# Performance work log

Hardware: AMD Instinct MI355X
Metric: run time of the kernel (lower is better)

Reference implementation:

```python
import jax, jax.numpy as jnp
import numpy as np

EPS = 1e-5

def _bn_relu(x, g, b, m, v):
    # inference batchnorm + relu, NCHW, fused affine
    scale = g * jax.lax.rsqrt(v + EPS)
    shift = b - m * scale
    return jnp.maximum(x * scale[None, :, None, None] + shift[None, :, None, None], 0.0)

def _conv1x1(x, w):
    # x: [B,C,H,W], w: [O,C]
    return jnp.einsum('bchw,oc->bohw', x, w)

def _xcorr_depthwise(search, kernel, padding=0):
    # search: [B,C,Hs,Ws], kernel: [B,C,Hk,Wk]; grouped conv, groups=B*C
    B, C, Hs, Ws = search.shape
    Hk, Wk = kernel.shape[2], kernel.shape[3]
    x = search.reshape(1, B * C, Hs, Ws)
    k = kernel.reshape(B * C, 1, Hk, Wk)
    out = jax.lax.conv_general_dilated(
        x, k, window_strides=(1, 1), padding=[(padding, padding), (padding, padding)],
        feature_group_count=B * C, dimension_numbers=('NCHW', 'OIHW', 'NCHW'))
    return out.reshape(B, C, out.shape[2], out.shape[3])

def setup_inputs():
    key = jax.random.key(0)
    ks = jax.random.split(key, 20)
    B, Cin, HID, COUT = 128, 256, 256, 20
    s = 1.0 / np.sqrt(Cin)
    inp = {
        'kernel': jax.random.normal(ks[0], (B, Cin, 7, 7), jnp.float32),
        'search': jax.random.normal(ks[1], (B, Cin, 31, 31), jnp.float32),
        # conv_kernel branch (1x1 conv weight stored as [O,C]) + BN stats
        'w_k': jax.random.normal(ks[2], (HID, Cin), jnp.float32) * s,
        'g_k': 1.0 + 0.1 * jax.random.normal(ks[3], (HID,), jnp.float32),
        'b_k': 0.1 * jax.random.normal(ks[4], (HID,), jnp.float32),
        'm_k': 0.1 * jax.random.normal(ks[5], (HID,), jnp.float32),
        'v_k': jax.random.uniform(ks[6], (HID,), jnp.float32, 0.5, 1.5),
        # conv_search branch
        'w_s': jax.random.normal(ks[7], (HID, Cin), jnp.float32) * s,
        'g_s': 1.0 + 0.1 * jax.random.normal(ks[8], (HID,), jnp.float32),
        'b_s': 0.1 * jax.random.normal(ks[9], (HID,), jnp.float32),
        'm_s': 0.1 * jax.random.normal(ks[10], (HID,), jnp.float32),
        'v_s': jax.random.uniform(ks[11], (HID,), jnp.float32, 0.5, 1.5),
        # head: conv1(1x1)+BN+ReLU, conv2(1x1, bias)
        'w_h1': jax.random.normal(ks[12], (HID, HID), jnp.float32) * (1.0 / np.sqrt(HID)),
        'g_h': 1.0 + 0.1 * jax.random.normal(ks[13], (HID,), jnp.float32),
        'b_h': 0.1 * jax.random.normal(ks[14], (HID,), jnp.float32),
        'm_h': 0.1 * jax.random.normal(ks[15], (HID,), jnp.float32),
        'v_h': jax.random.uniform(ks[16], (HID,), jnp.float32, 0.5, 1.5),
        'w_h2': jax.random.normal(ks[17], (COUT, HID), jnp.float32) * (1.0 / np.sqrt(HID)),
        'bias_h2': 0.1 * jax.random.normal(ks[18], (COUT,), jnp.float32),
    }
    return inp

def reference(kernel, search, w_k, g_k, b_k, m_k, v_k, w_s, g_s, b_s, m_s, v_s,
              w_h1, g_h, b_h, m_h, v_h, w_h2, bias_h2):
    k = _bn_relu(_conv1x1(kernel, w_k), g_k, b_k, m_k, v_k)   # [B,256,7,7]
    s = _bn_relu(_conv1x1(search, w_s), g_s, b_s, m_s, v_s)   # [B,256,31,31]
    feat = _xcorr_depthwise(s, k, padding=0)                  # [B,256,25,25]
    y = _bn_relu(_conv1x1(feat, w_h1), g_h, b_h, m_h, v_h)
    out = _conv1x1(y, w_h2) + bias_h2[None, :, None, None]    # [B,20,25,25]
    return out
```

## Files before the change

### kernel.cpp

```cpp
#include <hip/hip_runtime.h>
#include <hip/hip_fp16.h>

typedef _Float16 f16;
typedef __attribute__((ext_vector_type(8))) _Float16 f16x8;
typedef __attribute__((ext_vector_type(4))) _Float16 f16x4;
typedef __attribute__((ext_vector_type(4))) float f32x4;

#define MFMA16(a, b, c) __builtin_amdgcn_mfma_f32_16x16x32_f16((a), (b), (c), 0, 0, 0)

#define OFF_WK   0u
#define OFF_WS   131072u
#define OFF_WH1  262144u
#define OFF_W2P  393216u
#define OFF_SH   409600u
#define OFF_S    412672u
#define OFF_KF   63392768u
#define OFF_FEAT 66604032u

__global__ __launch_bounds__(256) void prep_weights(
    const float* __restrict__ wk, const float* __restrict__ gk, const float* __restrict__ bk,
    const float* __restrict__ mk, const float* __restrict__ vk,
    const float* __restrict__ wsr, const float* __restrict__ gs, const float* __restrict__ bs,
    const float* __restrict__ ms, const float* __restrict__ vs,
    const float* __restrict__ wh1, const float* __restrict__ gh, const float* __restrict__ bh,
    const float* __restrict__ mh, const float* __restrict__ vh,
    const float* __restrict__ wh2,
    f16* __restrict__ wk16, f16* __restrict__ ws16, f16* __restrict__ wh116,
    f16* __restrict__ w2p, float* __restrict__ shifts) {
  int o = blockIdx.x;
  int t = threadIdx.x;
  float sck = gk[o] * rsqrtf(vk[o] + 1e-5f);
  float scs = gs[o] * rsqrtf(vs[o] + 1e-5f);
  float sch = gh[o] * rsqrtf(vh[o] + 1e-5f);
  int idx = o * 256 + t;
  wk16[idx]  = (f16)(wk[idx] * sck);
  ws16[idx]  = (f16)(wsr[idx] * scs);
  wh116[idx] = (f16)(wh1[idx] * sch);
  if (o < 32) w2p[idx] = (o < 20) ? (f16)wh2[idx] : (f16)0;
  if (t == 0) {
    shifts[o]       = bk[o] - mk[o] * sck;
    shifts[256 + o] = bs[o] - ms[o] * scs;
    shifts[512 + o] = bh[o] - mh[o] * sch;
  }
}

__global__ __launch_bounds__(256) void conv_f32_allo(
    const float* __restrict__ X, const f16* __restrict__ W,
    const float* __restrict__ shift, f16* __restrict__ out,
    int P, int CP ) {
  const int C = 256;
  int n0 = blockIdx.x * 64;
  int t = threadIdx.x;
  int lane = t & 63, wave = t >> 6;
  int fm = lane & 15, kg = lane >> 4;

  __shared__ f16 Bs[32][64][8];

  {
    int n = t & 63;
    int cblk = t >> 6;
    int gn = n0 + n;
    int bq = gn / P, bp = gn - bq * P;
    const float* xcol = X + (size_t)bq * CP + bp;
#pragma unroll
    for (int j = 0; j < 8; ++j) {
      int cbase = cblk * 64 + j * 8;
      const float* xp = xcol + (size_t)cbase * P;
      f16x8 v;
#pragma unroll
      for (int e = 0; e < 8; ++e) v[e] = (f16)xp[(size_t)e * P];
      *(f16x8*)&Bs[cbase >> 3][n][0] = v;
    }
  }
  __syncthreads();

  const f16* wp = W + (size_t)(wave * 64 + fm) * C + kg * 8;

  f32x4 acc[4][4] = {};
#pragma unroll
  for (int c0 = 0; c0 < 256; c0 += 32) {
    f16x8 a[4], b[4];
#pragma unroll
    for (int of = 0; of < 4; ++of) a[of] = *(const f16x8*)(wp + (size_t)of * 16 * C + c0);
#pragma unroll
    for (int nf = 0; nf < 4; ++nf) b[nf] = *(const f16x8*)&Bs[(c0 >> 3) + kg][nf * 16 + fm][0];
#pragma unroll
    for (int of = 0; of < 4; ++of)
#pragma unroll
      for (int nf = 0; nf < 4; ++nf)
        acc[of][nf] = MFMA16(a[of], b[nf], acc[of][nf]);
  }

#pragma unroll
  for (int of = 0; of < 4; ++of) {
    int orow = wave * 64 + of * 16 + kg * 4;
#pragma unroll
    for (int nf = 0; nf < 4; ++nf) {
      int n = n0 + nf * 16 + fm;
      f16x4 st;
#pragma unroll
      for (int r = 0; r < 4; ++r)
        st[r] = (f16)fmaxf(acc[of][nf][r] + shift[orow + r], 0.0f);
      *(f16x4*)&out[(size_t)n * 256 + orow] = st;
    }
  }
}

__global__ __launch_bounds__(256) void xcorr_dw_row(
    const f16* __restrict__ S ,
    const f16* __restrict__ K ,
    f16* __restrict__ F ) {
  int id = blockIdx.x;
  int x = id & 7;
  int r = id >> 3;
  int g = r % 7;
  int bq = r / 7;
  int b = bq * 8 + x;

  int wave = threadIdx.x >> 6;
  int lane = threadIdx.x & 63;
  int oi = g * 4 + wave;
  if (oi >= 25) return;

  const f16* Sb = S + (size_t)b * 961 * 256 + lane * 4;
  const f16* Kb = K + (size_t)b * 49 * 256 + lane * 4;

  f32x4 acc[25] = {};

  for (int di = 0; di < 7; ++di) {
    const f16* sp = Sb + (size_t)(oi + di) * 31 * 256;
    f16x4 srow[31];
#pragma unroll
    for (int j = 0; j < 31; ++j) srow[j] = *(const f16x4*)(sp + (size_t)j * 256);
    const f16* kp = Kb + (size_t)di * 7 * 256;
    f16x4 krow[7];
#pragma unroll
    for (int j = 0; j < 7; ++j) krow[j] = *(const f16x4*)(kp + (size_t)j * 256);

#pragma unroll
    for (int dj = 0; dj < 7; ++dj) {
      float k0 = (float)krow[dj][0];
      float k1 = (float)krow[dj][1];
      float k2 = (float)krow[dj][2];
      float k3 = (float)krow[dj][3];
#pragma unroll
      for (int oj = 0; oj < 25; ++oj) {
        f16x4 sv = srow[oj + dj];
        acc[oj][0] += (float)sv[0] * k0;
        acc[oj][1] += (float)sv[1] * k1;
        acc[oj][2] += (float)sv[2] * k2;
        acc[oj][3] += (float)sv[3] * k3;
      }
    }
  }

  f16* Fb = F + ((size_t)b * 625 + (size_t)oi * 25) * 256 + lane * 4;
#pragma unroll
  for (int oj = 0; oj < 25; ++oj) {
    f16x4 o;
#pragma unroll
    for (int e = 0; e < 4; ++e) o[e] = (f16)acc[oj][e];
    *(f16x4*)(Fb + (size_t)oj * 256) = o;
  }
}

__global__ __launch_bounds__(256) void head_fused(
    const f16* __restrict__ Xt ,
    const f16* __restrict__ W1, const float* __restrict__ shift,
    const f16* __restrict__ W2p , const float* __restrict__ bias,
    float* __restrict__ out ) {
  const int C = 256;
  int n0 = blockIdx.x * 64;
  int t = threadIdx.x;
  int lane = t & 63, wave = t >> 6;
  int fm = lane & 15, kg = lane >> 4;

  __shared__ f16 Ys[32][64][8];

  const f16* wp = W1 + (size_t)(wave * 64 + fm) * C + kg * 8;
  const f16* xp = Xt + (size_t)(n0 + fm) * C + kg * 8;

  f32x4 acc[4][4] = {};
#pragma unroll
  for (int c0 = 0; c0 < 256; c0 += 32) {
    f16x8 a[4], b[4];
#pragma unroll
    for (int of = 0; of < 4; ++of) a[of] = *(const f16x8*)(wp + (size_t)of * 16 * C + c0);
#pragma unroll
    for (int nf = 0; nf < 4; ++nf) b[nf] = *(const f16x8*)(xp + (size_t)nf * 16 * C + c0);
#pragma unroll
    for (int of = 0; of < 4; ++of)
#pragma unroll
      for (int nf = 0; nf < 4; ++nf)
        acc[of][nf] = MFMA16(a[of], b[nf], acc[of][nf]);
  }

#pragma unroll
  for (int of = 0; of < 4; ++of) {
    int orow = wave * 64 + of * 16 + kg * 4;
#pragma unroll
    for (int nf = 0; nf < 4; ++nf) {
      int n = nf * 16 + fm;
      f16x4 st;
#pragma unroll
      for (int r = 0; r < 4; ++r)
        st[r] = (f16)fmaxf(acc[of][nf][r] + shift[orow + r], 0.0f);
      *(f16x4*)&Ys[orow >> 3][n][(kg & 1) * 4] = st;
    }
  }
  __syncthreads();

  f32x4 acc2[2] = {};
#pragma unroll
  for (int c0 = 0; c0 < 256; c0 += 32) {
    f16x8 b = *(const f16x8*)&Ys[(c0 >> 3) + kg][wave * 16 + fm][0];
    f16x8 a0 = *(const f16x8*)(W2p + (size_t)fm * C + c0 + kg * 8);
    f16x8 a1 = *(const f16x8*)(W2p + (size_t)(16 + fm) * C + c0 + kg * 8);
    acc2[0] = MFMA16(a0, b, acc2[0]);
    acc2[1] = MFMA16(a1, b, acc2[1]);
  }

  int n = n0 + wave * 16 + fm;
  int bq = n / 625, bp = n - bq * 625;
  float* op = out + (size_t)bq * 12500 + bp;
#pragma unroll
  for (int of = 0; of < 2; ++of) {
#pragma unroll
    for (int r = 0; r < 4; ++r) {
      int o = of * 16 + kg * 4 + r;
      if (o < 20) op[(size_t)o * 625] = acc2[of][r] + bias[o];
    }
  }
}

extern "C" void kernel_launch(void* const* d_in, const int* in_sizes, int n_in,
                              void* d_out, int out_size, void* d_ws, size_t ws_size,
                              hipStream_t stream) {
  const float* kernel_in = (const float*)d_in[0];
  const float* search    = (const float*)d_in[1];
  const float* w_k = (const float*)d_in[2];
  const float* g_k = (const float*)d_in[3];
  const float* b_k = (const float*)d_in[4];
  const float* m_k = (const float*)d_in[5];
  const float* v_k = (const float*)d_in[6];
  const float* w_s = (const float*)d_in[7];
  const float* g_s = (const float*)d_in[8];
  const float* b_s = (const float*)d_in[9];
  const float* m_s = (const float*)d_in[10];
  const float* v_s = (const float*)d_in[11];
  const float* w_h1 = (const float*)d_in[12];
  const float* g_h = (const float*)d_in[13];
  const float* b_h = (const float*)d_in[14];
  const float* m_h = (const float*)d_in[15];
  const float* v_h = (const float*)d_in[16];
  const float* w_h2 = (const float*)d_in[17];
  const float* bias_h2 = (const float*)d_in[18];
  float* out = (float*)d_out;

  char* ws = (char*)d_ws;
  f16* wk16  = (f16*)(ws + OFF_WK);
  f16* ws16  = (f16*)(ws + OFF_WS);
  f16* wh116 = (f16*)(ws + OFF_WH1);
  f16* w2p   = (f16*)(ws + OFF_W2P);
  float* shifts = (float*)(ws + OFF_SH);
  f16* sbuf = (f16*)(ws + OFF_S);
  f16* kbuf = (f16*)(ws + OFF_KF);
  f16* fbuf = (f16*)(ws + OFF_FEAT);

  prep_weights<<<256, 256, 0, stream>>>(w_k, g_k, b_k, m_k, v_k,
                                        w_s, g_s, b_s, m_s, v_s,
                                        w_h1, g_h, b_h, m_h, v_h, w_h2,
                                        wk16, ws16, wh116, w2p, shifts);

  conv_f32_allo<<<dim3(1922), 256, 0, stream>>>(
      search, ws16, shifts + 256, sbuf, 961, 256 * 961);

  conv_f32_allo<<<dim3(98), 256, 0, stream>>>(
      kernel_in, wk16, shifts + 0, kbuf, 49, 256 * 49);

  xcorr_dw_row<<<dim3(896), 256, 0, stream>>>(sbuf, kbuf, fbuf);

  head_fused<<<dim3(1250), 256, 0, stream>>>(
      fbuf, wh116, shifts + 512, w2p, bias_h2, out);
}
```

Measured before the change: 184.0 us.

## Split 1x1 conv into channel-last f16 transpose plus in-place MFMA GEMM

Replaces the fused f32-load-and-convert 1x1 conv with two steps. A templated transpose kernel converts NCHW f32 input to channel-last f16 using vectorized loads. A GEMM kernel then reads the channel-last data straight from global memory without LDS staging, uses a wider 128-column tile and writes its result in place. The aim is cheaper, more coalesced loads and better MFMA reuse, but it adds an extra write and read of the intermediate f16 tensor in global memory.

Measured after the change: 216.4 us. +17.6%, slower.

```diff
diff --git a/kernel.cpp b/kernel.cpp
--- a/kernel.cpp
+++ b/kernel.cpp
@@ -44,64 +44,83 @@
   }
 }
 
-__global__ __launch_bounds__(256) void conv_f32_allo(
-    const float* __restrict__ X, const f16* __restrict__ W,
-    const float* __restrict__ shift, f16* __restrict__ out,
-    int P, int CP ) {
+template <int P>
+__global__ __launch_bounds__(256) void transpose_cl(
+    const float* __restrict__ X, f16* __restrict__ out) {
+  int p0 = blockIdx.x * 128;
+  int c0 = blockIdx.y * 64;
+  int b  = blockIdx.z;
+  int t = threadIdx.x;
+  int cg = t & 7;
+  int pq = t >> 3;
+  int p = p0 + pq * 4;
+  if (p >= P) return;
+  const float* xb = X + ((size_t)b * 256 + c0 + cg * 8) * P;
+  f32x4 col[8];
+  if (p + 3 < P) {
+#pragma unroll
+    for (int j = 0; j < 8; ++j) col[j] = *(const f32x4*)(xb + (size_t)j * P + p);
+  } else {
+#pragma unroll
+    for (int j = 0; j < 8; ++j)
+#pragma unroll
+      for (int e = 0; e < 4; ++e)
+        col[j][e] = (p + e < P) ? xb[(size_t)j * P + p + e] : 0.0f;
+  }
+#pragma unroll
+  for (int e = 0; e < 4; ++e) {
+    if (p + e < P) {
+      f16x8 v;
+#pragma unroll
+      for (int j = 0; j < 8; ++j) v[j] = (f16)col[j][e];
+      *(f16x8*)(out + ((size_t)b * P + p + e) * 256 + c0 + cg * 8) = v;
+    }
+  }
+}
+
+__global__ __launch_bounds__(256, 2) void gemm_cl(
+    const f16* Xt, const f16* __restrict__ W,
+    const float* __restrict__ shift, f16* out) {
   const int C = 256;
-  int n0 = blockIdx.x * 64;
+  int n0 = blockIdx.x * 128;
   int t = threadIdx.x;
   int lane = t & 63, wave = t >> 6;
   int fm = lane & 15, kg = lane >> 4;
 
-  __shared__ f16 Bs[32][64][8];
-
-  {
-    int n = t & 63;
-    int cblk = t >> 6;
-    int gn = n0 + n;
-    int bq = gn / P, bp = gn - bq * P;
-    const float* xcol = X + (size_t)bq * CP + bp;
-#pragma unroll
-    for (int j = 0; j < 8; ++j) {
-      int cbase = cblk * 64 + j * 8;
-      const float* xp = xcol + (size_t)cbase * P;
-      f16x8 v;
-#pragma unroll
-      for (int e = 0; e < 8; ++e) v[e] = (f16)xp[(size_t)e * P];
-      *(f16x8*)&Bs[cbase >> 3][n][0] = v;
-    }
-  }
+  const f16* wp = W + (size_t)(wave * 64 + fm) * C + kg * 8;
+  const f16* xp = Xt + (size_t)(n0 + fm) * C + kg * 8;
+
+  f32x4 acc[4][8] = {};
+#pragma unroll
+  for (int ci = 0; ci < 8; ++ci) {
+    f16x8 b[8], a[4];
+#pragma unroll
+    for (int nf = 0; nf < 8; ++nf)
+      b[nf] = *(const f16x8*)(xp + (size_t)nf * 16 * C + ci * 32);
+#pragma unroll
+    for (int of = 0; of < 4; ++of)
+      a[of] = *(const f16x8*)(wp + (size_t)of * 16 * C + ci * 32);
+#pragma unroll
+    for (int of = 0; of < 4; ++of)
+#pragma unroll
+      for (int nf = 0; nf < 8; ++nf)
+        acc[of][nf] = MFMA16(a[of], b[nf], acc[of][nf]);
+  }
+
   __syncthreads();
-
-  const f16* wp = W + (size_t)(wave * 64 + fm) * C + kg * 8;
-
-  f32x4 acc[4][4] = {};
-#pragma unroll
-  for (int c0 = 0; c0 < 256; c0 += 32) {
-    f16x8 a[4], b[4];
-#pragma unroll
-    for (int of = 0; of < 4; ++of) a[of] = *(const f16x8*)(wp + (size_t)of * 16 * C + c0);
-#pragma unroll
-    for (int nf = 0; nf < 4; ++nf) b[nf] = *(const f16x8*)&Bs[(c0 >> 3) + kg][nf * 16 + fm][0];
-#pragma unroll
-    for (int of = 0; of < 4; ++of)
-#pragma unroll
-      for (int nf = 0; nf < 4; ++nf)
-        acc[of][nf] = MFMA16(a[of], b[nf], acc[of][nf]);
-  }
 
 #pragma unroll
   for (int of = 0; of < 4; ++of) {
     int orow = wave * 64 + of * 16 + kg * 4;
-#pragma unroll
-    for (int nf = 0; nf < 4; ++nf) {
+    f32x4 sh = *(const f32x4*)(shift + orow);
+#pragma unroll
+    for (int nf = 0; nf < 8; ++nf) {
       int n = n0 + nf * 16 + fm;
       f16x4 st;
 #pragma unroll
       for (int r = 0; r < 4; ++r)
-        st[r] = (f16)fmaxf(acc[of][nf][r] + shift[orow + r], 0.0f);
-      *(f16x4*)&out[(size_t)n * 256 + orow] = st;
+        st[r] = (f16)fmaxf(acc[of][nf][r] + sh[r], 0.0f);
+      *(f16x4*)(out + (size_t)n * C + orow) = st;
     }
   }
 }
@@ -272,11 +291,11 @@
                                         w_h1, g_h, b_h, m_h, v_h, w_h2,
                                         wk16, ws16, wh116, w2p, shifts);
 
-  conv_f32_allo<<<dim3(1922), 256, 0, stream>>>(
-      search, ws16, shifts + 256, sbuf, 961, 256 * 961);
-
-  conv_f32_allo<<<dim3(98), 256, 0, stream>>>(
-      kernel_in, wk16, shifts + 0, kbuf, 49, 256 * 49);
+  transpose_cl<961><<<dim3(8, 4, 128), 256, 0, stream>>>(search, sbuf);
+  transpose_cl<49><<<dim3(1, 4, 128), 256, 0, stream>>>(kernel_in, kbuf);
+
+  gemm_cl<<<dim3(961), 256, 0, stream>>>(sbuf, ws16, shifts + 256, sbuf);
+  gemm_cl<<<dim3(49), 256, 0, stream>>>(kbuf, wk16, shifts + 0, kbuf);
 
   xcorr_dw_row<<<dim3(896), 256, 0, stream>>>(sbuf, kbuf, fbuf);
 
```

## Retile 1x1 input convs to 16-pixel per-batch blocks with vectorized fp32 staging

Applied to the files above, without the earlier changes.

Replaces the generic 64-column conv kernel with a templated one where each block covers 16 pixels of a single batch image. Each block loads the fp32 input as float4 rows into padded shared memory and converts to fp16 while forming the MFMA B operand. The last tile in each image is clamped, so some pixels are computed twice. This drops the per-pixel batch division and scalar strided loads and gives many more blocks, but each block reuses the weight tile 4x less, which adds weight traffic from L2.

Result: slower. 253.7 us (+37.9%).

```diff
diff --git a/kernel.cpp b/kernel.cpp
--- a/kernel.cpp
+++ b/kernel.cpp
@@ -44,65 +44,64 @@
   }
 }
 
-__global__ __launch_bounds__(256) void conv_f32_allo(
+template <int P>
+__global__ __launch_bounds__(256) void conv_px16(
     const float* __restrict__ X, const f16* __restrict__ W,
-    const float* __restrict__ shift, f16* __restrict__ out,
-    int P, int CP ) {
+    const float* __restrict__ shift, f16* __restrict__ out) {
   const int C = 256;
-  int n0 = blockIdx.x * 64;
+  int p0 = blockIdx.x * 16;
+  if (p0 > P - 16) p0 = P - 16;
+  int b = blockIdx.y;
   int t = threadIdx.x;
   int lane = t & 63, wave = t >> 6;
   int fm = lane & 15, kg = lane >> 4;
 
-  __shared__ f16 Bs[32][64][8];
-
-  {
-    int n = t & 63;
-    int cblk = t >> 6;
-    int gn = n0 + n;
-    int bq = gn / P, bp = gn - bq * P;
-    const float* xcol = X + (size_t)bq * CP + bp;
-#pragma unroll
-    for (int j = 0; j < 8; ++j) {
-      int cbase = cblk * 64 + j * 8;
-      const float* xp = xcol + (size_t)cbase * P;
-      f16x8 v;
-#pragma unroll
-      for (int e = 0; e < 8; ++e) v[e] = (f16)xp[(size_t)e * P];
-      *(f16x8*)&Bs[cbase >> 3][n][0] = v;
-    }
+  __shared__ float Xs[256 * 17];
+
+  const float* xb = X + (size_t)b * C * P + p0;
+  int c0 = t >> 2, q = t & 3;
+  f32x4 v[4];
+#pragma unroll
+  for (int it = 0; it < 4; ++it)
+    v[it] = *(const f32x4*)(xb + (size_t)(it * 64 + c0) * P + q * 4);
+#pragma unroll
+  for (int it = 0; it < 4; ++it) {
+    int c = it * 64 + c0;
+#pragma unroll
+    for (int e = 0; e < 4; ++e)
+      Xs[c * 17 + q * 4 + e] = v[it][e];
   }
   __syncthreads();
 
   const f16* wp = W + (size_t)(wave * 64 + fm) * C + kg * 8;
 
-  f32x4 acc[4][4] = {};
-#pragma unroll
-  for (int c0 = 0; c0 < 256; c0 += 32) {
-    f16x8 a[4], b[4];
-#pragma unroll
-    for (int of = 0; of < 4; ++of) a[of] = *(const f16x8*)(wp + (size_t)of * 16 * C + c0);
-#pragma unroll
-    for (int nf = 0; nf < 4; ++nf) b[nf] = *(const f16x8*)&Bs[(c0 >> 3) + kg][nf * 16 + fm][0];
+  f32x4 acc[4] = {};
+#pragma unroll
+  for (int ci = 0; ci < 8; ++ci) {
+    f16x8 a[4];
 #pragma unroll
     for (int of = 0; of < 4; ++of)
-#pragma unroll
-      for (int nf = 0; nf < 4; ++nf)
-        acc[of][nf] = MFMA16(a[of], b[nf], acc[of][nf]);
-  }
-
+      a[of] = *(const f16x8*)(wp + (size_t)of * 16 * C + ci * 32);
+    int cb = ci * 32 + kg * 8;
+    f16x8 bf;
+#pragma unroll
+    for (int j = 0; j < 8; ++j)
+      bf[j] = (f16)Xs[(cb + j) * 17 + fm];
+#pragma unroll
+    for (int of = 0; of < 4; ++of)
+      acc[of] = MFMA16(a[of], bf, acc[of]);
+  }
+
+  size_t n = (size_t)b * P + p0 + fm;
 #pragma unroll
   for (int of = 0; of < 4; ++of) {
     int orow = wave * 64 + of * 16 + kg * 4;
-#pragma unroll
-    for (int nf = 0; nf < 4; ++nf) {
-      int n = n0 + nf * 16 + fm;
-      f16x4 st;
-#pragma unroll
-      for (int r = 0; r < 4; ++r)
-        st[r] = (f16)fmaxf(acc[of][nf][r] + shift[orow + r], 0.0f);
-      *(f16x4*)&out[(size_t)n * 256 + orow] = st;
-    }
+    f32x4 sh = *(const f32x4*)(shift + orow);
+    f16x4 st;
+#pragma unroll
+    for (int r = 0; r < 4; ++r)
+      st[r] = (f16)fmaxf(acc[of][r] + sh[r], 0.0f);
+    *(f16x4*)(out + n * C + orow) = st;
   }
 }
 
@@ -272,11 +271,8 @@
                                         w_h1, g_h, b_h, m_h, v_h, w_h2,
                                         wk16, ws16, wh116, w2p, shifts);
 
-  conv_f32_allo<<<dim3(1922), 256, 0, stream>>>(
-      search, ws16, shifts + 256, sbuf, 961, 256 * 961);
-
-  conv_f32_allo<<<dim3(98), 256, 0, stream>>>(
-      kernel_in, wk16, shifts + 0, kbuf, 49, 256 * 49);
+  conv_px16<961><<<dim3(61, 128), 256, 0, stream>>>(search, ws16, shifts + 256, sbuf);
+  conv_px16<49><<<dim3(4, 128), 256, 0, stream>>>(kernel_in, wk16, shifts + 0, kbuf);
 
   xcorr_dw_row<<<dim3(896), 256, 0, stream>>>(sbuf, kbuf, fbuf);
 
```
